# Kernel optimization log

Hardware: AMD Instinct MI355X
Metric: run time of the kernel (lower is better)

The kernel has to match this reference:

```python
import jax, jax.numpy as jnp
import numpy as np

B, L, K = 256, 128, 6
FA, FB, D = 39, 10, 128
R, T = 3, 2
NEG = -9e8


def _gru(x, h, wih, whh, bih, bhh):
    # torch.nn.GRUCell semantics
    gi = x @ wih.T + bih
    gh = h @ whh.T + bhh
    ir, iz, inn = jnp.split(gi, 3, axis=-1)
    hr, hz, hn = jnp.split(gh, 3, axis=-1)
    r = jax.nn.sigmoid(ir + hr)
    z = jax.nn.sigmoid(iz + hz)
    n = jnp.tanh(inn + r * hn)
    return (1.0 - z) * n + z * h


def _forward(atom_list, bond_list, atom_mask, atom_fc_w, atom_fc_b, nbr_fc_w, nbr_fc_b,
             align_w, align_b, attend_w, attend_b, gru_wih, gru_whh, gru_bih, gru_bhh,
             mol_align_w, mol_align_b, mol_attend_w, mol_attend_b,
             mol_gru_wih, mol_gru_whh, mol_gru_bih, mol_gru_bhh, out_w, out_b,
             atom_degree_list, bond_degree_list):
    lrelu = jax.nn.leaky_relu  # slope 0.01, matches torch default
    bidx = jnp.arange(atom_list.shape[0])[:, None, None]
    gather = lambda f, idx: f[bidx, idx]  # [B,L,F] gathered by [B,L,K] -> [B,L,K,F]

    atom_feature = lrelu(atom_list @ atom_fc_w + atom_fc_b)  # [B,L,D]
    nbr = jnp.concatenate([gather(atom_list, atom_degree_list),
                           gather(bond_list, bond_degree_list)], axis=-1)
    nbr = lrelu(nbr @ nbr_fc_w + nbr_fc_b)  # [B,L,K,D]

    pad = atom_list.shape[1] - 1  # mol_length-1 is padding sentinel
    attend_mask = (atom_degree_list != pad).astype(atom_feature.dtype)[..., None]
    softmax_mask = jnp.where(atom_degree_list == pad, NEG, 0.0).astype(atom_feature.dtype)[..., None]

    def attn(cur, nbr_feat, aw, ab, tw, tb):
        exp = jnp.broadcast_to(cur[:, :, None, :], nbr_feat.shape)
        score = lrelu(jnp.concatenate([exp, nbr_feat], axis=-1) @ aw + ab) + softmax_mask
        w = jax.nn.softmax(score, axis=-2) * attend_mask  # softmax over neighbors
        return jax.nn.elu(jnp.sum(w * (nbr_feat @ tw + tb), axis=-2))

    h = atom_feature
    ctx = attn(atom_feature, nbr, align_w[0], align_b[0], attend_w[0], attend_b[0])
    h = _gru(ctx, h, gru_wih[0], gru_whh[0], gru_bih[0], gru_bhh[0])
    act = jax.nn.relu(h)
    for d in range(1, R):
        nbr_f = gather(act, atom_degree_list)
        ctx = attn(act, nbr_f, align_w[d], align_b[d], attend_w[d], attend_b[d])
        h = _gru(ctx, h, gru_wih[d], gru_whh[d], gru_bih[d], gru_bhh[d])
        act = jax.nn.relu(h)

    am = atom_mask[..., None]  # [B,L,1]
    mol_feature = jnp.sum(act * am, axis=-2)  # [B,D]
    act_mol = jax.nn.relu(mol_feature)
    mol_smask = jnp.where(am == 0, NEG, 0.0).astype(atom_feature.dtype)
    for _ in range(T):
        exp = jnp.broadcast_to(act_mol[:, None, :], act.shape)
        score = lrelu(jnp.concatenate([exp, act], axis=-1) @ mol_align_w + mol_align_b) + mol_smask
        w = jax.nn.softmax(score, axis=-2) * am  # softmax over atoms
        ctx = jax.nn.elu(jnp.sum(w * (act @ mol_attend_w + mol_attend_b), axis=-2))
        mol_feature = _gru(ctx, mol_feature, mol_gru_wih, mol_gru_whh, mol_gru_bih, mol_gru_bhh)
        act_mol = jax.nn.relu(mol_feature)
    mol_prediction = mol_feature @ out_w + out_b  # [B,1]
    return h, mol_prediction


def setup_inputs():
    key = jax.random.key(0)
    ks = jax.random.split(key, 30)
    f = lambda i, s: jax.random.normal(ks[i], s, dtype=jnp.float32) * 0.1
    return {
        'atom_list': jax.random.normal(ks[0], (B, L, FA), dtype=jnp.float32),
        'bond_list': jax.random.normal(ks[1], (B, L, FB), dtype=jnp.float32),
        'atom_mask': jnp.ones((B, L), jnp.float32),
        'atom_fc_w': f(2, (FA, D)), 'atom_fc_b': f(3, (D,)),
        'nbr_fc_w': f(4, (FA + FB, D)), 'nbr_fc_b': f(5, (D,)),
        'align_w': f(6, (R, 2 * D, 1)), 'align_b': f(7, (R, 1)),
        'attend_w': f(8, (R, D, D)), 'attend_b': f(9, (R, D)),
        'gru_wih': f(10, (R, 3 * D, D)), 'gru_whh': f(11, (R, 3 * D, D)),
        'gru_bih': f(12, (R, 3 * D)), 'gru_bhh': f(13, (R, 3 * D)),
        'mol_align_w': f(14, (2 * D, 1)), 'mol_align_b': f(15, (1,)),
        'mol_attend_w': f(16, (D, D)), 'mol_attend_b': f(17, (D,)),
        'mol_gru_wih': f(18, (3 * D, D)), 'mol_gru_whh': f(19, (3 * D, D)),
        'mol_gru_bih': f(20, (3 * D,)), 'mol_gru_bhh': f(21, (3 * D,)),
        'out_w': f(22, (D, 1)), 'out_b': f(23, (1,)),
        'atom_degree_list': jax.random.randint(ks[24], (B, L, K), 0, L),
        'bond_degree_list': jax.random.randint(ks[25], (B, L, K), 0, L),
    }


def reference(atom_list, bond_list, atom_mask, atom_fc_w, atom_fc_b, nbr_fc_w, nbr_fc_b,
              align_w, align_b, attend_w, attend_b, gru_wih, gru_whh, gru_bih, gru_bhh,
              mol_align_w, mol_align_b, mol_attend_w, mol_attend_b,
              mol_gru_wih, mol_gru_whh, mol_gru_bih, mol_gru_bhh, out_w, out_b,
              atom_degree_list, bond_degree_list):
    return _forward(atom_list, bond_list, atom_mask, atom_fc_w, atom_fc_b, nbr_fc_w, nbr_fc_b,
                    align_w, align_b, attend_w, attend_b, gru_wih, gru_whh, gru_bih, gru_bhh,
                    mol_align_w, mol_align_b, mol_attend_w, mol_attend_b,
                    mol_gru_wih, mol_gru_whh, mol_gru_bih, mol_gru_bhh, out_w, out_b,
                    atom_degree_list, bond_degree_list)
```

## Files before the change

### kernel.cpp

```cpp
#include <hip/hip_runtime.h>
#include <cstddef>


#define B_ 256
#define L_ 128
#define K_ 6
#define FA_ 39
#define FB_ 10
#define D_ 128
#define PAD_ 127
#define NEGC (-9.0e8f)
#define NA 16
#define NPAIR (NA * K_)

typedef unsigned short u16;
typedef unsigned int u32;
using s8 = __attribute__((ext_vector_type(8))) short;
using f4 = __attribute__((ext_vector_type(4))) float;

#define WIH_H 0
#define WIH_L 49152
#define WHH_H 98304
#define WHH_L 147456
#define TW_H  196608
#define TW_L  212992
#define RND_BLK2 229376
#define NB16 (3 * RND_BLK2)
#define NMOLF (2 * 128 * 384)

__device__ __forceinline__ float lrelu(float x) { return x > 0.f ? x : 0.01f * x; }
__device__ __forceinline__ float eluf(float x)  { return x > 0.f ? x : expm1f(x); }
__device__ __forceinline__ float sigm(float x)  { return 1.f / (1.f + expf(-x)); }
__device__ __forceinline__ float b2f(u16 u) {
  union { u32 i; float f; } v; v.i = ((u32)u) << 16; return v.f;
}
__device__ __forceinline__ short f2b(float f) {
  union { float f; u32 i; } v; v.f = f;
  u32 x = v.i;
  return (short)(u16)((x + 0x7FFFu + ((x >> 16) & 1u)) >> 16);
}

__global__ __launch_bounds__(256) void k_tr(
    const float* __restrict__ gwih, const float* __restrict__ gwhh,
    const float* __restrict__ attw,
    const float* __restrict__ mwih, const float* __restrict__ mwhh,
    short* __restrict__ wB, float* __restrict__ molT) {
  int idx = blockIdx.x * 256 + threadIdx.x;
  if (idx < NB16) {
    int r = idx / RND_BLK2, o = idx % RND_BLK2;
    float v; int lo;
    int e, kind;
    if (o < 98304)      { kind = 0; lo = o / 49152; e = o % 49152; }
    else if (o < 196608){ kind = 1; int o2 = o - 98304; lo = o2 / 49152; e = o2 % 49152; }
    else                { kind = 2; int o2 = o - 196608; lo = o2 / 16384; e = o2 % 16384; }
    int gt = e >> 11, rem = e & 2047;
    int kc = rem >> 9, rem2 = rem & 511;
    int lane = rem2 >> 3, j = rem2 & 7;
    int col = lane & 15, quad = lane >> 4;
    int g = gt * 16 + col;
    int k = kc * 32 + quad * 8 + j;
    if (kind == 0)      v = gwih[(size_t)r * 49152 + g * 128 + k];
    else if (kind == 1) v = gwhh[(size_t)r * 49152 + g * 128 + k];
    else                v = attw[(size_t)r * 16384 + k * 128 + g];
    short hi = f2b(v);
    wB[idx] = lo ? f2b(v - b2f((u16)hi)) : hi;
  } else if (idx < NB16 + NMOLF) {
    int e2 = idx - NB16;
    int m = e2 / 49152, e = e2 % 49152, j = e / 384, g = e % 384;
    molT[e2] = (m ? mwhh : mwih)[g * 128 + j];
  }
}

__global__ __launch_bounds__(128) void k_pre(
    const float* __restrict__ atom_list,
    const float* __restrict__ afc_w, const float* __restrict__ afc_b,
    const float* __restrict__ nbr_w,
    const float* __restrict__ aw0,
    u16* __restrict__ h0out, short* __restrict__ APg, float* __restrict__ PgA)
{
  int tid = threadIdx.x;
  int a0 = blockIdx.x * 16;
  __shared__ float xa[16 * 40];
  __shared__ float h0S[16][132];
  __shared__ float awS[128];
  __shared__ float partials[128];

  for (int i = tid; i < 16 * FA_; i += 128) {
    int a = i / FA_, c = i % FA_;
    xa[a * 40 + c] = atom_list[((size_t)(a0 + a)) * FA_ + c];
  }
  awS[tid] = aw0[tid];
  __syncthreads();

  {
    float acc[16];
    float bv = afc_b[tid];
#pragma unroll
    for (int a = 0; a < 16; a++) acc[a] = bv;
#pragma unroll 2
    for (int j = 0; j < FA_; j++) {
      float w = afc_w[j * D_ + tid];
#pragma unroll
      for (int a = 0; a < 16; a++) acc[a] += xa[a * 40 + j] * w;
    }
#pragma unroll
    for (int a = 0; a < 16; a++) {
      float hv = lrelu(acc[a]);
      h0out[(size_t)(a0 + a) * D_ + tid] = (u16)f2b(hv);
      h0S[a][tid] = hv;
    }
  }
  {
    float acc[16];
#pragma unroll
    for (int a = 0; a < 16; a++) acc[a] = 0.f;
#pragma unroll 2
    for (int j = 0; j < FA_; j++) {
      float w = nbr_w[j * D_ + tid];
#pragma unroll
      for (int a = 0; a < 16; a++) acc[a] += xa[a * 40 + j] * w;
    }
#pragma unroll
    for (int a = 0; a < 16; a++)
      APg[(size_t)(a0 + a) * D_ + tid] = f2b(acc[a]);
  }
  __syncthreads();
  {
    int a = tid >> 3, seg = tid & 7;
    float s = 0.f;
#pragma unroll
    for (int j = 0; j < 16; j++) s += h0S[a][seg * 16 + j] * awS[seg * 16 + j];
    partials[tid] = s;
  }
  __syncthreads();
  if (tid < 16) {
    float s = 0.f;
#pragma unroll
    for (int g = 0; g < 8; g++) s += partials[tid * 8 + g];
    PgA[a0 + tid] = s;
  }
}

__global__ __launch_bounds__(256) void k_q0(
    const float* __restrict__ bond_list,
    const float* __restrict__ nbr_w, const float* __restrict__ nbr_b,
    const float* __restrict__ aw0,
    const int* __restrict__ adeg, const int* __restrict__ bdeg,
    const short* __restrict__ APg, float* __restrict__ Q0g)
{
  int tid = threadIdx.x;
  __shared__ float WbS[10 * 128];
  __shared__ float nbS[128], ahS[128];
  for (int i = tid; i < 10 * 128; i += 256)
    WbS[i] = nbr_w[(FA_ + i / 128) * D_ + (i % 128)];
  if (tid < 128) { nbS[tid] = nbr_b[tid]; ahS[tid] = aw0[D_ + tid]; }
  __syncthreads();

  int p = blockIdx.x * 64 + (tid >> 2);
  int seg = tid & 3;
  int aidx = adeg[p], bidx = bdeg[p];
  int bb = p / (L_ * K_);
  const short* rowA = APg + ((size_t)bb * L_ + aidx) * D_;
  const float* brow = bond_list + ((size_t)bb * L_ + bidx) * FB_;
  float bnd[10];
#pragma unroll
  for (int m = 0; m < 10; m++) bnd[m] = brow[m];
  float s = 0.f;
  int j0 = seg * 32;
#pragma unroll 4
  for (int j = j0; j < j0 + 32; j++) {
    float v = b2f((u16)rowA[j]) + nbS[j];
#pragma unroll
    for (int m = 0; m < 10; m++) v += bnd[m] * WbS[m * 128 + j];
    s += lrelu(v) * ahS[j];
  }
  s += __shfl_xor(s, 1, 64);
  s += __shfl_xor(s, 2, 64);
  if (seg == 0) Q0g[p] = s;
}

template <int FIRST>
__global__ __launch_bounds__(256, 6) void k_round(
    const u16* __restrict__ hin,
    u16* __restrict__ hout,
    const float* __restrict__ bond_list,
    const int* __restrict__ adeg, const int* __restrict__ bdeg,
    const float* __restrict__ nbr_w, const float* __restrict__ nbr_b,
    const short* __restrict__ APg,
    const float* __restrict__ ab,
    const float* __restrict__ awN,
    const float* __restrict__ tb,
    const short* __restrict__ wR,
    const float* __restrict__ bih, const float* __restrict__ bhh,
    const float* __restrict__ Pr, const float* __restrict__ Qr,
    float* __restrict__ Pw, float* __restrict__ Qw)
{
  int tid  = threadIdx.x;
  int t128 = tid & 127;
  int hf   = tid >> 7;
  int lane = tid & 63;
  int wv   = tid >> 6;
  int quad = lane >> 4;
  int col  = lane & 15;
  int a0   = blockIdx.x * NA;
  int bb   = a0 >> 7;

  const short* wihH = wR + WIH_H;
  const short* wihL = wR + WIH_L;
  const short* whhH = wR + WHH_H;
  const short* whhL = wR + WHH_L;
  const short* twH  = wR + TW_H;
  const short* twL  = wR + TW_L;

  __shared__ short hrowH[NA][136];
  __shared__ __align__(16) char arena[9472];
  __shared__ float awNS[256];
  __shared__ float partials[256];
  __shared__ float pS[NA], qS[NPAIR], wkS[NPAIR], wsS[NA];
  __shared__ int aidxS[NPAIR];
  __shared__ int bidxS[FIRST ? NPAIR : 1];
  __shared__ float bwS[FIRST ? 2368 : 1];

  short* ybarH = (short*)arena;
  short* ybarL = (short*)(arena + 4352);
  float* hnrel = (float*)arena;

  if (tid < NPAIR) {
    int av = adeg[a0 * K_ + tid];
    aidxS[tid] = av;
    if (FIRST) { bidxS[tid] = bdeg[a0 * K_ + tid]; qS[tid] = Qr[a0 * K_ + tid]; }
    else       qS[tid] = Qr[bb * L_ + av];
  } else if (tid >= 128 && tid < 128 + NA) {
    pS[tid - 128] = Pr[a0 + (tid - 128)];
  }
  awNS[tid] = awN[tid];
  __syncthreads();

  if (FIRST) {
    for (int i = tid; i < 960; i += 256) {
      int p = i / 10, m = i % 10;
      bwS[p * 10 + m] = bond_list[((size_t)bb * L_ + bidxS[p]) * FB_ + m];
    }
    for (int i = tid; i < 1280; i += 256)
      bwS[960 + i] = nbr_w[(FA_ + i / 128) * D_ + (i % 128)];
    if (tid < 128) bwS[2240 + tid] = nbr_b[tid];
  }
#pragma unroll 4
  for (int i = 0; i < 8; i++) {
    int a = i * 2 + hf;
    hrowH[a][t128] = (short)hin[(size_t)(a0 + a) * D_ + t128];
  }
  __syncthreads();

  if (tid < NA) {
    int a = tid;
    float abv = ab[0];
    float sc[K_];
    float m = -3.0e38f;
#pragma unroll
    for (int k = 0; k < K_; k++) {
      float s = lrelu(pS[a] + qS[a * K_ + k] + abv);
      if (aidxS[a * K_ + k] == PAD_) s += NEGC;
      sc[k] = s; m = fmaxf(m, s);
    }
    float es = 0.f;
#pragma unroll
    for (int k = 0; k < K_; k++) { sc[k] = expf(sc[k] - m); es += sc[k]; }
    float ws = 0.f;
#pragma unroll
    for (int k = 0; k < K_; k++) {
      float w = (aidxS[a * K_ + k] == PAD_) ? 0.f : sc[k] / es;
      wkS[a * K_ + k] = w; ws += w;
    }
    wsS[a] = ws;
  }
  __syncthreads();

  if (FIRST) {
    const float* bondS = bwS;
    const float* WbS   = bwS + 960;
    float nbv = bwS[2240 + t128];
#pragma unroll
    for (int i = 0; i < 8; i++) {
      int a = hf * 8 + i;
      float yb = 0.f;
#pragma unroll
      for (int k = 0; k < K_; k++) {
        int p = a * K_ + k;
        float nf = b2f((u16)APg[((size_t)bb * L_ + aidxS[p]) * D_ + t128]) + nbv;
#pragma unroll
        for (int m = 0; m < 10; m++) nf += bondS[p * 10 + m] * WbS[m * 128 + t128];
        yb += wkS[p] * lrelu(nf);
      }
      short yh = f2b(yb);
      ybarH[a * 136 + t128] = yh;
      ybarL[a * 136 + t128] = f2b(yb - b2f((u16)yh));
    }
  } else {
#pragma unroll
    for (int i = 0; i < 8; i++) {
      int a = hf * 8 + i;
      float yb = 0.f;
#pragma unroll
      for (int k = 0; k < K_; k++) {
        float v = b2f(hin[((size_t)bb * L_ + aidxS[a * K_ + k]) * D_ + t128]);
        yb += wkS[a * K_ + k] * fmaxf(v, 0.f);
      }
      short yh = f2b(yb);
      ybarH[a * 136 + t128] = yh;
      ybarL[a * 136 + t128] = f2b(yb - b2f((u16)yh));
    }
  }
  __syncthreads();

  {
    f4 c2[2] = {};
#pragma unroll
    for (int k0c = 0; k0c < 4; k0c++) {
      s8 ayh = *(const s8*)&ybarH[col * 136 + k0c * 32 + quad * 8];
      s8 ayl = *(const s8*)&ybarL[col * 136 + k0c * 32 + quad * 8];
#pragma unroll
      for (int t = 0; t < 2; t++) {
        int gt = 2 * wv + t;
        int fo = ((gt * 4 + k0c) * 64 + lane) * 8;
        s8 bwh = *(const s8*)&twH[fo];
        s8 bwl = *(const s8*)&twL[fo];
        c2[t] = __builtin_amdgcn_mfma_f32_16x16x32_bf16(ayh, bwh, c2[t], 0, 0, 0);
        c2[t] = __builtin_amdgcn_mfma_f32_16x16x32_bf16(ayl, bwh, c2[t], 0, 0, 0);
        c2[t] = __builtin_amdgcn_mfma_f32_16x16x32_bf16(ayh, bwl, c2[t], 0, 0, 0);
      }
    }
    __syncthreads();
#pragma unroll
    for (int t = 0; t < 2; t++) {
      int g = (2 * wv + t) * 16 + col;
      float tbv = tb[g];
#pragma unroll
      for (int r = 0; r < 4; r++) {
        int a = quad * 4 + r;
        float c = eluf(c2[t][r] + wsS[a] * tbv);
        short chs = f2b(c);
        ybarH[a * 136 + g] = chs;
        ybarL[a * 136 + g] = f2b(c - b2f((u16)chs));
      }
    }
  }
  __syncthreads();

  {
    const short* ctxH = ybarH;
    const short* ctxL = ybarL;
    f4 gi[2][3] = {}, gh[2][3] = {};
#pragma unroll
    for (int k0c = 0; k0c < 4; k0c++) {
      s8 ach = *(const s8*)&ctxH[col * 136 + k0c * 32 + quad * 8];
      s8 acl = *(const s8*)&ctxL[col * 136 + k0c * 32 + quad * 8];
      s8 ahh = *(const s8*)&hrowH[col][k0c * 32 + quad * 8];
#pragma unroll
      for (int t = 0; t < 2; t++) {
#pragma unroll
        for (int kd = 0; kd < 3; kd++) {
          int gt = (2 * wv + t) + kd * 8;
          int fo = ((gt * 4 + k0c) * 64 + lane) * 8;
          s8 bi_h = *(const s8*)&wihH[fo];
          s8 bi_l = *(const s8*)&wihL[fo];
          s8 bh_h = *(const s8*)&whhH[fo];
          s8 bh_l = *(const s8*)&whhL[fo];
          gi[t][kd] = __builtin_amdgcn_mfma_f32_16x16x32_bf16(ach, bi_h, gi[t][kd], 0, 0, 0);
          gi[t][kd] = __builtin_amdgcn_mfma_f32_16x16x32_bf16(acl, bi_h, gi[t][kd], 0, 0, 0);
          gi[t][kd] = __builtin_amdgcn_mfma_f32_16x16x32_bf16(ach, bi_l, gi[t][kd], 0, 0, 0);
          gh[t][kd] = __builtin_amdgcn_mfma_f32_16x16x32_bf16(ahh, bh_h, gh[t][kd], 0, 0, 0);
          gh[t][kd] = __builtin_amdgcn_mfma_f32_16x16x32_bf16(ahh, bh_l, gh[t][kd], 0, 0, 0);
        }
      }
    }
    __syncthreads();

#pragma unroll
    for (int t = 0; t < 2; t++) {
      int ic = (2 * wv + t) * 16 + col;
      float bi0 = bih[ic], bi1 = bih[D_ + ic], bi2 = bih[2 * D_ + ic];
      float bh0 = bhh[ic], bh1 = bhh[D_ + ic], bh2 = bhh[2 * D_ + ic];
#pragma unroll
      for (int r = 0; r < 4; r++) {
        int a = quad * 4 + r;
        float rr = sigm(gi[t][0][r] + bi0 + gh[t][0][r] + bh0);
        float zz = sigm(gi[t][1][r] + bi1 + gh[t][1][r] + bh1);
        float nn = tanhf(gi[t][2][r] + bi2 + rr * (gh[t][2][r] + bh2));
        float hv = b2f((u16)hrowH[a][ic]);
        float hn = (1.f - zz) * nn + zz * hv;
        hout[(size_t)(a0 + a) * D_ + ic] = (u16)f2b(hn);
        if (Pw) hnrel[a * 132 + ic] = fmaxf(hn, 0.f);
      }
    }
  }

  if (Pw) {
    __syncthreads();
    {
      int a = tid >> 4, dt = (tid >> 3) & 1, seg = tid & 7;
      float s = 0.f;
#pragma unroll
      for (int j = 0; j < 16; j++)
        s += hnrel[a * 132 + seg * 16 + j] * awNS[dt * 128 + seg * 16 + j];
      partials[tid] = s;
    }
    __syncthreads();
    if (tid < 32) {
      int a = tid >> 1, dt = tid & 1;
      float s = 0.f;
#pragma unroll
      for (int seg = 0; seg < 8; seg++) s += partials[a * 16 + dt * 8 + seg];
      if (dt) Qw[a0 + a] = s; else Pw[a0 + a] = s;
    }
  }
}

__global__ __launch_bounds__(512) void k_mol(
    const u16* __restrict__ hfin,
    float* __restrict__ hcopy,
    const float* __restrict__ amask,
    const float* __restrict__ maw, const float* __restrict__ mab,
    const float* __restrict__ mtw, const float* __restrict__ mtb,
    const float* __restrict__ wih_t, const float* __restrict__ whh_t,
    const float* __restrict__ bih, const float* __restrict__ bhh,
    const float* __restrict__ ow, const float* __restrict__ ob,
    float* __restrict__ pred)
{
  int b = blockIdx.x;
  int tid = threadIdx.x;
  int t128 = tid & 127;
  int qf = tid >> 7;
  __shared__ float actS[L_][D_ + 1];
  __shared__ float red[512];
  __shared__ float par4[4][132];
  __shared__ float pg[3][6][132];
  __shared__ float wgt[128], ybv[132], ctx[132], mfS[132], amol[132];
  __shared__ float msk[128], mawh[128], scf[128];

  if (qf == 0) { msk[t128] = amask[b * L_ + t128]; mawh[t128] = maw[D_ + t128]; }
  for (int i = 0; i < 32; i++) {
    int l = qf * 32 + i;
    float hv = b2f(hfin[(size_t)(b * L_ + l) * D_ + t128]);
    hcopy[(size_t)(b * L_ + l) * D_ + t128] = hv;
    actS[l][t128] = fmaxf(hv, 0.f);
  }
  __syncthreads();

  {
    float s = 0.f;
    for (int i = 0; i < 32; i++) { int l = qf * 32 + i; s += actS[l][t128] * msk[l]; }
    par4[qf][t128] = s;
  }
  __syncthreads();
  if (qf == 0) {
    float mf = par4[0][t128] + par4[1][t128] + par4[2][t128] + par4[3][t128];
    mfS[t128] = mf; amol[t128] = fmaxf(mf, 0.f);
  }
  __syncthreads();

  float mabv = mab[0];

  for (int t = 0; t < 2; t++) {
    red[tid] = (tid < 128) ? amol[tid] * maw[tid] : 0.f;
    __syncthreads();
    for (int s = 256; s > 0; s >>= 1) { if (tid < s) red[tid] += red[tid + s]; __syncthreads(); }
    float s0 = red[0]; __syncthreads();

    {
      float s = 0.f;
      for (int i = 0; i < 32; i++) { int j = qf * 32 + i; s += actS[t128][j] * mawh[j]; }
      par4[qf][t128] = s;
    }
    __syncthreads();
    if (qf == 0) {
      float sc = lrelu(s0 + mabv + par4[0][t128] + par4[1][t128] + par4[2][t128] + par4[3][t128]);
      if (msk[t128] == 0.f) sc += NEGC;
      scf[t128] = sc;
    }
    __syncthreads();

    float scv = scf[t128];
    red[tid] = (tid < 128) ? scv : -3.0e38f;
    __syncthreads();
    for (int s = 256; s > 0; s >>= 1) { if (tid < s) red[tid] = fmaxf(red[tid], red[tid + s]); __syncthreads(); }
    float mx = red[0]; __syncthreads();
    float e = expf(scv - mx);
    red[tid] = (tid < 128) ? e : 0.f;
    __syncthreads();
    for (int s = 256; s > 0; s >>= 1) { if (tid < s) red[tid] += red[tid + s]; __syncthreads(); }
    float es = red[0]; __syncthreads();
    float w = (e / es) * msk[t128];
    if (qf == 0) wgt[t128] = w;
    red[tid] = (tid < 128) ? w : 0.f;
    __syncthreads();
    for (int s = 256; s > 0; s >>= 1) { if (tid < s) red[tid] += red[tid + s]; __syncthreads(); }
    float wsum = red[0]; __syncthreads();

    {
      float s = 0.f;
      for (int i = 0; i < 32; i++) { int l = qf * 32 + i; s += wgt[l] * actS[l][t128]; }
      par4[qf][t128] = s;
    }
    __syncthreads();
    if (qf == 0) ybv[t128] = par4[0][t128] + par4[1][t128] + par4[2][t128] + par4[3][t128];
    __syncthreads();

    {
      float s = 0.f;
#pragma unroll 2
      for (int i = 0; i < 32; i++) { int j = qf * 32 + i; s += ybv[j] * mtw[j * D_ + t128]; }
      par4[qf][t128] = s;
    }
    __syncthreads();
    if (qf == 0)
      ctx[t128] = eluf(par4[0][t128] + par4[1][t128] + par4[2][t128] + par4[3][t128]
                       + wsum * mtb[t128]);
    __syncthreads();

    {
      float gi0 = 0, gi1 = 0, gi2 = 0, gh0 = 0, gh1 = 0, gh2 = 0;
#pragma unroll 2
      for (int i = 0; i < 32; i++) {
        int j = qf * 32 + i;
        const float* wi = wih_t + (size_t)j * 384;
        const float* wh = whh_t + (size_t)j * 384;
        float xc = ctx[j], xh = mfS[j];
        gi0 += xc * wi[t128]; gi1 += xc * wi[128 + t128]; gi2 += xc * wi[256 + t128];
        gh0 += xh * wh[t128]; gh1 += xh * wh[128 + t128]; gh2 += xh * wh[256 + t128];
      }
      if (qf > 0) {
        pg[qf - 1][0][t128] = gi0; pg[qf - 1][1][t128] = gi1; pg[qf - 1][2][t128] = gi2;
        pg[qf - 1][3][t128] = gh0; pg[qf - 1][4][t128] = gh1; pg[qf - 1][5][t128] = gh2;
      }
      __syncthreads();
      if (qf == 0) {
        gi0 += pg[0][0][t128] + pg[1][0][t128] + pg[2][0][t128] + bih[t128];
        gi1 += pg[0][1][t128] + pg[1][1][t128] + pg[2][1][t128] + bih[128 + t128];
        gi2 += pg[0][2][t128] + pg[1][2][t128] + pg[2][2][t128] + bih[256 + t128];
        gh0 += pg[0][3][t128] + pg[1][3][t128] + pg[2][3][t128] + bhh[t128];
        gh1 += pg[0][4][t128] + pg[1][4][t128] + pg[2][4][t128] + bhh[128 + t128];
        gh2 += pg[0][5][t128] + pg[1][5][t128] + pg[2][5][t128] + bhh[256 + t128];
        float r = sigm(gi0 + gh0);
        float z = sigm(gi1 + gh1);
        float n = tanhf(gi2 + r * gh2);
        float hn = (1.f - z) * n + z * mfS[t128];
        mfS[t128] = hn;
        amol[t128] = fmaxf(hn, 0.f);
      }
      __syncthreads();
    }
  }

  red[tid] = (tid < 128) ? mfS[tid] * ow[tid] : 0.f;
  __syncthreads();
  for (int s = 256; s > 0; s >>= 1) { if (tid < s) red[tid] += red[tid + s]; __syncthreads(); }
  if (tid == 0) pred[b] = red[0] + ob[0];
}

extern "C" void kernel_launch(void* const* d_in, const int* in_sizes, int n_in,
                              void* d_out, int out_size, void* d_ws, size_t ws_size,
                              hipStream_t stream) {
  const float* atom_list    = (const float*)d_in[0];
  const float* bond_list    = (const float*)d_in[1];
  const float* atom_mask    = (const float*)d_in[2];
  const float* atom_fc_w    = (const float*)d_in[3];
  const float* atom_fc_b    = (const float*)d_in[4];
  const float* nbr_fc_w     = (const float*)d_in[5];
  const float* nbr_fc_b     = (const float*)d_in[6];
  const float* align_w      = (const float*)d_in[7];
  const float* align_b      = (const float*)d_in[8];
  const float* attend_w     = (const float*)d_in[9];
  const float* attend_b     = (const float*)d_in[10];
  const float* gru_wih      = (const float*)d_in[11];
  const float* gru_whh      = (const float*)d_in[12];
  const float* gru_bih      = (const float*)d_in[13];
  const float* gru_bhh      = (const float*)d_in[14];
  const float* mol_align_w  = (const float*)d_in[15];
  const float* mol_align_b  = (const float*)d_in[16];
  const float* mol_attend_w = (const float*)d_in[17];
  const float* mol_attend_b = (const float*)d_in[18];
  const float* mol_gru_wih  = (const float*)d_in[19];
  const float* mol_gru_whh  = (const float*)d_in[20];
  const float* mol_gru_bih  = (const float*)d_in[21];
  const float* mol_gru_bhh  = (const float*)d_in[22];
  const float* out_w        = (const float*)d_in[23];
  const float* out_b        = (const float*)d_in[24];
  const int*   adeg         = (const int*)d_in[25];
  const int*   bdeg         = (const int*)d_in[26];

  const size_t NH = (size_t)B_ * L_ * D_;
  u16*   hA   = (u16*)d_ws;
  u16*   hB   = hA + NH;
  short* wB   = (short*)(hB + NH);
  float* molT = (float*)(wB + NB16);
  float* PgA  = molT + NMOLF;
  float* QgA  = PgA + B_ * L_;
  float* PgB  = QgA + B_ * L_;
  float* QgB  = PgB + B_ * L_;
  short* APg  = (short*)(QgB + B_ * L_);
  float* Q0g  = (float*)(APg + NH);
  float* hOut = (float*)d_out;
  float* pred = hOut + NH;

  k_tr<<<dim3((NB16 + NMOLF + 255) / 256), dim3(256), 0, stream>>>(
      gru_wih, gru_whh, attend_w, mol_gru_wih, mol_gru_whh, wB, molT);

  k_pre<<<dim3(B_ * L_ / 16), dim3(128), 0, stream>>>(
      atom_list, atom_fc_w, atom_fc_b, nbr_fc_w, align_w, hA, APg, PgA);
  k_q0<<<dim3(B_ * L_ * K_ / 64), dim3(256), 0, stream>>>(
      bond_list, nbr_fc_w, nbr_fc_b, align_w, adeg, bdeg, APg, Q0g);

  dim3 blk(256), grd(B_ * L_ / NA);

  k_round<1><<<grd, blk, 0, stream>>>(
      hA, hB, bond_list, adeg, bdeg, nbr_fc_w, nbr_fc_b, APg,
      align_b, align_w + 2 * D_, attend_b,
      wB + 0 * (size_t)RND_BLK2, gru_bih, gru_bhh,
      PgA, Q0g, PgB, QgB);
  k_round<0><<<grd, blk, 0, stream>>>(
      hB, hA, bond_list, adeg, bdeg, nbr_fc_w, nbr_fc_b, APg,
      align_b + 1, align_w + 4 * D_, attend_b + D_,
      wB + 1 * (size_t)RND_BLK2, gru_bih + 3 * D_, gru_bhh + 3 * D_,
      PgB, QgB, PgA, QgA);
  k_round<0><<<grd, blk, 0, stream>>>(
      hA, hB, bond_list, adeg, bdeg, nbr_fc_w, nbr_fc_b, APg,
      align_b + 2, align_w + 4 * D_, attend_b + 2 * D_,
      wB + 2 * (size_t)RND_BLK2, gru_bih + 6 * D_, gru_bhh + 6 * D_,
      PgA, QgA, (float*)nullptr, (float*)nullptr);

  k_mol<<<dim3(B_), dim3(512), 0, stream>>>(
      hB, hOut, atom_mask, mol_align_w, mol_align_b, mol_attend_w, mol_attend_b,
      molT, molT + 128 * 384,
      mol_gru_bih, mol_gru_bhh, out_w, out_b, pred);
}
```

Before: 394.4 us.

## Process 32 atoms per round block with 512 threads to reuse weight fragments

Doubles the atoms per k_round block from 16 to 32 and the block size from 256 to 512 threads. Each wave now owns one 16-column output tile and loads each weight fragment once for two atom tiles, where before each 16-atom block reloaded every fragment. This halves global and L2 weight traffic per atom. In exchange it uses more shared memory and registers per block, and the launch bound of 512 threads with 6 blocks may force register spills or lower occupancy.

```diff
diff --git a/kernel.cpp b/kernel.cpp
--- a/kernel.cpp
+++ b/kernel.cpp
@@ -10,7 +10,7 @@
 #define D_ 128
 #define PAD_ 127
 #define NEGC (-9.0e8f)
-#define NA 16
+#define NA 32
 #define NPAIR (NA * K_)
 
 typedef unsigned short u16;
@@ -180,7 +180,7 @@
 }
 
 template <int FIRST>
-__global__ __launch_bounds__(256, 6) void k_round(
+__global__ __launch_bounds__(512, 6) void k_round(
     const u16* __restrict__ hin,
     u16* __restrict__ hout,
     const float* __restrict__ bond_list,
@@ -197,7 +197,7 @@
 {
   int tid  = threadIdx.x;
   int t128 = tid & 127;
-  int hf   = tid >> 7;
+  int hq   = tid >> 7;
   int lane = tid & 63;
   int wv   = tid >> 6;
   int quad = lane >> 4;
@@ -213,16 +213,16 @@
   const short* twL  = wR + TW_L;
 
   __shared__ short hrowH[NA][136];
-  __shared__ __align__(16) char arena[9472];
+  __shared__ __align__(16) char arena[17408];
   __shared__ float awNS[256];
-  __shared__ float partials[256];
+  __shared__ float partials[512];
   __shared__ float pS[NA], qS[NPAIR], wkS[NPAIR], wsS[NA];
   __shared__ int aidxS[NPAIR];
   __shared__ int bidxS[FIRST ? NPAIR : 1];
-  __shared__ float bwS[FIRST ? 2368 : 1];
+  __shared__ float bwS[FIRST ? 3328 : 1];
 
   short* ybarH = (short*)arena;
-  short* ybarL = (short*)(arena + 4352);
+  short* ybarL = (short*)(arena + 8704);
   float* hnrel = (float*)arena;
 
   if (tid < NPAIR) {
@@ -230,24 +230,24 @@
     aidxS[tid] = av;
     if (FIRST) { bidxS[tid] = bdeg[a0 * K_ + tid]; qS[tid] = Qr[a0 * K_ + tid]; }
     else       qS[tid] = Qr[bb * L_ + av];
-  } else if (tid >= 128 && tid < 128 + NA) {
-    pS[tid - 128] = Pr[a0 + (tid - 128)];
-  }
-  awNS[tid] = awN[tid];
+  } else if (tid < NPAIR + NA) {
+    pS[tid - NPAIR] = Pr[a0 + (tid - NPAIR)];
+  }
+  if (tid < 256) awNS[tid] = awN[tid];
   __syncthreads();
 
   if (FIRST) {
-    for (int i = tid; i < 960; i += 256) {
+    for (int i = tid; i < NPAIR * 10; i += 512) {
       int p = i / 10, m = i % 10;
       bwS[p * 10 + m] = bond_list[((size_t)bb * L_ + bidxS[p]) * FB_ + m];
     }
-    for (int i = tid; i < 1280; i += 256)
-      bwS[960 + i] = nbr_w[(FA_ + i / 128) * D_ + (i % 128)];
-    if (tid < 128) bwS[2240 + tid] = nbr_b[tid];
+    for (int i = tid; i < 1280; i += 512)
+      bwS[1920 + i] = nbr_w[(FA_ + i / 128) * D_ + (i % 128)];
+    if (tid < 128) bwS[3200 + tid] = nbr_b[tid];
   }
 #pragma unroll 4
   for (int i = 0; i < 8; i++) {
-    int a = i * 2 + hf;
+    int a = i * 4 + hq;
     hrowH[a][t128] = (short)hin[(size_t)(a0 + a) * D_ + t128];
   }
   __syncthreads();
@@ -278,11 +278,11 @@
 
   if (FIRST) {
     const float* bondS = bwS;
-    const float* WbS   = bwS + 960;
-    float nbv = bwS[2240 + t128];
+    const float* WbS   = bwS + 1920;
+    float nbv = bwS[3200 + t128];
 #pragma unroll
     for (int i = 0; i < 8; i++) {
-      int a = hf * 8 + i;
+      int a = hq * 8 + i;
       float yb = 0.f;
 #pragma unroll
       for (int k = 0; k < K_; k++) {
@@ -299,7 +299,7 @@
   } else {
 #pragma unroll
     for (int i = 0; i < 8; i++) {
-      int a = hf * 8 + i;
+      int a = hq * 8 + i;
       float yb = 0.f;
 #pragma unroll
       for (int k = 0; k < K_; k++) {
@@ -317,28 +317,27 @@
     f4 c2[2] = {};
 #pragma unroll
     for (int k0c = 0; k0c < 4; k0c++) {
-      s8 ayh = *(const s8*)&ybarH[col * 136 + k0c * 32 + quad * 8];
-      s8 ayl = *(const s8*)&ybarL[col * 136 + k0c * 32 + quad * 8];
-#pragma unroll
-      for (int t = 0; t < 2; t++) {
-        int gt = 2 * wv + t;
-        int fo = ((gt * 4 + k0c) * 64 + lane) * 8;
-        s8 bwh = *(const s8*)&twH[fo];
-        s8 bwl = *(const s8*)&twL[fo];
-        c2[t] = __builtin_amdgcn_mfma_f32_16x16x32_bf16(ayh, bwh, c2[t], 0, 0, 0);
-        c2[t] = __builtin_amdgcn_mfma_f32_16x16x32_bf16(ayl, bwh, c2[t], 0, 0, 0);
-        c2[t] = __builtin_amdgcn_mfma_f32_16x16x32_bf16(ayh, bwl, c2[t], 0, 0, 0);
-      }
-    }
-    __syncthreads();
-#pragma unroll
-    for (int t = 0; t < 2; t++) {
-      int g = (2 * wv + t) * 16 + col;
-      float tbv = tb[g];
+      int fo = ((wv * 4 + k0c) * 64 + lane) * 8;
+      s8 bwh = *(const s8*)&twH[fo];
+      s8 bwl = *(const s8*)&twL[fo];
+#pragma unroll
+      for (int at = 0; at < 2; at++) {
+        s8 ayh = *(const s8*)&ybarH[(at * 16 + col) * 136 + k0c * 32 + quad * 8];
+        s8 ayl = *(const s8*)&ybarL[(at * 16 + col) * 136 + k0c * 32 + quad * 8];
+        c2[at] = __builtin_amdgcn_mfma_f32_16x16x32_bf16(ayh, bwh, c2[at], 0, 0, 0);
+        c2[at] = __builtin_amdgcn_mfma_f32_16x16x32_bf16(ayl, bwh, c2[at], 0, 0, 0);
+        c2[at] = __builtin_amdgcn_mfma_f32_16x16x32_bf16(ayh, bwl, c2[at], 0, 0, 0);
+      }
+    }
+    __syncthreads();
+    int g = wv * 16 + col;
+    float tbv = tb[g];
+#pragma unroll
+    for (int at = 0; at < 2; at++) {
 #pragma unroll
       for (int r = 0; r < 4; r++) {
-        int a = quad * 4 + r;
-        float c = eluf(c2[t][r] + wsS[a] * tbv);
+        int a = at * 16 + quad * 4 + r;
+        float c = eluf(c2[at][r] + wsS[a] * tbv);
         short chs = f2b(c);
         ybarH[a * 136 + g] = chs;
         ybarL[a * 136 + g] = f2b(c - b2f((u16)chs));
@@ -353,44 +352,50 @@
     f4 gi[2][3] = {}, gh[2][3] = {};
 #pragma unroll
     for (int k0c = 0; k0c < 4; k0c++) {
-      s8 ach = *(const s8*)&ctxH[col * 136 + k0c * 32 + quad * 8];
-      s8 acl = *(const s8*)&ctxL[col * 136 + k0c * 32 + quad * 8];
-      s8 ahh = *(const s8*)&hrowH[col][k0c * 32 + quad * 8];
-#pragma unroll
-      for (int t = 0; t < 2; t++) {
-#pragma unroll
-        for (int kd = 0; kd < 3; kd++) {
-          int gt = (2 * wv + t) + kd * 8;
-          int fo = ((gt * 4 + k0c) * 64 + lane) * 8;
-          s8 bi_h = *(const s8*)&wihH[fo];
-          s8 bi_l = *(const s8*)&wihL[fo];
-          s8 bh_h = *(const s8*)&whhH[fo];
-          s8 bh_l = *(const s8*)&whhL[fo];
-          gi[t][kd] = __builtin_amdgcn_mfma_f32_16x16x32_bf16(ach, bi_h, gi[t][kd], 0, 0, 0);
-          gi[t][kd] = __builtin_amdgcn_mfma_f32_16x16x32_bf16(acl, bi_h, gi[t][kd], 0, 0, 0);
-          gi[t][kd] = __builtin_amdgcn_mfma_f32_16x16x32_bf16(ach, bi_l, gi[t][kd], 0, 0, 0);
-          gh[t][kd] = __builtin_amdgcn_mfma_f32_16x16x32_bf16(ahh, bh_h, gh[t][kd], 0, 0, 0);
-          gh[t][kd] = __builtin_amdgcn_mfma_f32_16x16x32_bf16(ahh, bh_l, gh[t][kd], 0, 0, 0);
+      s8 ach[2], acl[2], ahh[2];
+#pragma unroll
+      for (int at = 0; at < 2; at++) {
+        ach[at] = *(const s8*)&ctxH[(at * 16 + col) * 136 + k0c * 32 + quad * 8];
+        acl[at] = *(const s8*)&ctxL[(at * 16 + col) * 136 + k0c * 32 + quad * 8];
+        ahh[at] = *(const s8*)&hrowH[at * 16 + col][k0c * 32 + quad * 8];
+      }
+#pragma unroll
+      for (int kd = 0; kd < 3; kd++) {
+        int gt = wv + kd * 8;
+        int fo = ((gt * 4 + k0c) * 64 + lane) * 8;
+        s8 bi_h = *(const s8*)&wihH[fo];
+        s8 bi_l = *(const s8*)&wihL[fo];
+        s8 bh_h = *(const s8*)&whhH[fo];
+        s8 bh_l = *(const s8*)&whhL[fo];
+#pragma unroll
+        for (int at = 0; at < 2; at++) {
+          gi[at][kd] = __builtin_amdgcn_mfma_f32_16x16x32_bf16(ach[at], bi_h, gi[at][kd], 0, 0, 0);
+          gi[at][kd] = __builtin_amdgcn_mfma_f32_16x16x32_bf16(acl[at], bi_h, gi[at][kd], 0, 0, 0);
+          gi[at][kd] = __builtin_amdgcn_mfma_f32_16x16x32_bf16(ach[at], bi_l, gi[at][kd], 0, 0, 0);
+          gh[at][kd] = __builtin_amdgcn_mfma_f32_16x16x32_bf16(ahh[at], bh_h, gh[at][kd], 0, 0, 0);
+          gh[at][kd] = __builtin_amdgcn_mfma_f32_16x16x32_bf16(ahh[at], bh_l, gh[at][kd], 0, 0, 0);
         }
       }
     }
     __syncthreads();
 
-#pragma unroll
-    for (int t = 0; t < 2; t++) {
-      int ic = (2 * wv + t) * 16 + col;
+    {
+      int ic = wv * 16 + col;
       float bi0 = bih[ic], bi1 = bih[D_ + ic], bi2 = bih[2 * D_ + ic];
       float bh0 = bhh[ic], bh1 = bhh[D_ + ic], bh2 = bhh[2 * D_ + ic];
 #pragma unroll
-      for (int r = 0; r < 4; r++) {
-        int a = quad * 4 + r;
-        float rr = sigm(gi[t][0][r] + bi0 + gh[t][0][r] + bh0);
-        float zz = sigm(gi[t][1][r] + bi1 + gh[t][1][r] + bh1);
-        float nn = tanhf(gi[t][2][r] + bi2 + rr * (gh[t][2][r] + bh2));
-        float hv = b2f((u16)hrowH[a][ic]);
-        float hn = (1.f - zz) * nn + zz * hv;
-        hout[(size_t)(a0 + a) * D_ + ic] = (u16)f2b(hn);
-        if (Pw) hnrel[a * 132 + ic] = fmaxf(hn, 0.f);
+      for (int at = 0; at < 2; at++) {
+#pragma unroll
+        for (int r = 0; r < 4; r++) {
+          int a = at * 16 + quad * 4 + r;
+          float rr = sigm(gi[at][0][r] + bi0 + gh[at][0][r] + bh0);
+          float zz = sigm(gi[at][1][r] + bi1 + gh[at][1][r] + bh1);
+          float nn = tanhf(gi[at][2][r] + bi2 + rr * (gh[at][2][r] + bh2));
+          float hv = b2f((u16)hrowH[a][ic]);
+          float hn = (1.f - zz) * nn + zz * hv;
+          hout[(size_t)(a0 + a) * D_ + ic] = (u16)f2b(hn);
+          if (Pw) hnrel[a * 132 + ic] = fmaxf(hn, 0.f);
+        }
       }
     }
   }
@@ -406,7 +411,7 @@
       partials[tid] = s;
     }
     __syncthreads();
-    if (tid < 32) {
+    if (tid < 64) {
       int a = tid >> 1, dt = tid & 1;
       float s = 0.f;
 #pragma unroll
@@ -611,7 +616,7 @@
   k_q0<<<dim3(B_ * L_ * K_ / 64), dim3(256), 0, stream>>>(
       bond_list, nbr_fc_w, nbr_fc_b, align_w, adeg, bdeg, APg, Q0g);
 
-  dim3 blk(256), grd(B_ * L_ / NA);
+  dim3 blk(512), grd(B_ * L_ / NA);
 
   k_round<1><<<grd, blk, 0, stream>>>(
       hA, hB, bond_list, adeg, bdeg, nbr_fc_w, nbr_fc_b, APg,
```

Result: faster. 370.2 us (-6.1%).
